# Kernel optimization log

Measured on AMD Instinct MI355X. Metric: run time of the kernel, lower is better.

## Reference

```python
import jax, jax.numpy as jnp
import numpy as np

N = 50000      # number of graph nodes (square sparse matrix)
NNZ = 800000   # nonzeros: avg degree 16
D = 256        # feature dim of m


def setup_inputs() -> dict:
    key = jax.random.key(0)
    k1, k2, k3, k4 = jax.random.split(key, 4)
    m = jax.random.normal(k1, (N, D), dtype=jnp.float32)
    # COO coordinates of the sparse graph matrix; row sorted to mimic CSR layout
    row = jnp.sort(jax.random.randint(k2, (NNZ,), 0, N))
    col = jax.random.randint(k3, (NNZ,), 0, N)
    vals = jax.random.normal(k4, (NNZ,), dtype=jnp.float32)
    return {"m": m, "row": row, "col": col, "vals": vals}


def reference(m, row, col, vals):
    # Faithful to NaiveMerge.forward: cast input to fp16 (self.dtype),
    # SpMM with the fp16 CSR matrix, then cast back to input dtype.
    H = m.astype(jnp.float16)                    # [N, D] fp16
    v = vals.astype(jnp.float16)                 # [NNZ] fp16 (matrix stored in self.dtype)
    msgs = H[col] * v[:, None]                   # [NNZ, D] gathered, scaled messages
    out = jax.ops.segment_sum(msgs, row, num_segments=N)  # CSR row-wise reduce -> [N, D]
    return out.astype(m.dtype)
```

## Files before the change

kernel.cpp:

```cpp
#include <hip/hip_runtime.h>
#include <hip/hip_fp16.h>


#define D   256
#define D4  64
#define D8  32

__device__ __forceinline__ int lower_bound_dev(const int* __restrict__ a, int n, int key) {
    int lo = 0, hi = n;
    while (lo < hi) {
        int mid = (lo + hi) >> 1;
        if (a[mid] < key) lo = mid + 1;
        else hi = mid;
    }
    return lo;
}

__global__ __launch_bounds__(256) void prep_kernel(
        const float4* __restrict__ m4,
        const int* __restrict__ row,
        int nnz, int n_rows,
        uint4* __restrict__ mh_vec,
        int* __restrict__ row_ptr) {
    const int tid = blockIdx.x * blockDim.x + threadIdx.x;
    const int nth = gridDim.x * blockDim.x;

    const int n_items = n_rows * D8;
    for (int i = tid; i < n_items; i += nth) {
        const float4 a = m4[2 * i];
        const float4 b = m4[2 * i + 1];
        union { __half h[8]; uint4 u; } pk;
        pk.h[0] = __float2half(a.x); pk.h[1] = __float2half(a.y);
        pk.h[2] = __float2half(a.z); pk.h[3] = __float2half(a.w);
        pk.h[4] = __float2half(b.x); pk.h[5] = __float2half(b.y);
        pk.h[6] = __float2half(b.z); pk.h[7] = __float2half(b.w);
        mh_vec[i] = pk.u;
    }

    for (int r = tid; r <= n_rows; r += nth) {
        row_ptr[r] = lower_bound_dev(row, nnz, r);
    }
}

__global__ __launch_bounds__(256) void spmm_fp16_kernel(
        const __half* __restrict__ mh,
        const int* __restrict__ row_ptr,
        const int* __restrict__ col,
        const float* __restrict__ vals,
        float4* __restrict__ out4,
        int n_rows) {
    const int wid  = threadIdx.x >> 6;
    const int lane = threadIdx.x & 63;
    const int r = blockIdx.x * 4 + wid;
    if (r >= n_rows) return;

    const int start = __builtin_amdgcn_readfirstlane(row_ptr[r]);
    const int end   = __builtin_amdgcn_readfirstlane(row_ptr[r + 1]);

    const uint2* __restrict__ mh2 = (const uint2*)mh;

    float a0 = 0.f, a1 = 0.f, a2 = 0.f, a3 = 0.f;

    for (int e0 = start; e0 < end; e0 += 16) {
        int   c[16];
        float v[16];
        if (e0 + 16 <= end) {
            #pragma unroll
            for (int j = 0; j < 16; ++j) {
                c[j] = col[e0 + j];
                v[j] = vals[e0 + j];
            }
        } else {
            const int last = end - 1;
            #pragma unroll
            for (int j = 0; j < 16; ++j) {
                const int e  = e0 + j;
                const int ec = e < end ? e : last;
                c[j] = col[ec];
                const float vv = vals[ec];
                v[j] = e < end ? vv : 0.f;
            }
        }

        uint2 g[16];
        #pragma unroll
        for (int j = 0; j < 16; ++j) {
            g[j] = mh2[((size_t)c[j] << 6) + lane];
        }

        __builtin_amdgcn_sched_barrier(0);

        __half2 s01a = __float2half2_rn(0.f);
        __half2 s23a = __float2half2_rn(0.f);
        __half2 s01b = __float2half2_rn(0.f);
        __half2 s23b = __float2half2_rn(0.f);
        #pragma unroll
        for (int j = 0; j < 16; j += 2) {
            const __half2 hva = __float2half2_rn(v[j]);
            s01a = __hfma2(__builtin_bit_cast(__half2, g[j].x), hva, s01a);
            s23a = __hfma2(__builtin_bit_cast(__half2, g[j].y), hva, s23a);
            const __half2 hvb = __float2half2_rn(v[j + 1]);
            s01b = __hfma2(__builtin_bit_cast(__half2, g[j + 1].x), hvb, s01b);
            s23b = __hfma2(__builtin_bit_cast(__half2, g[j + 1].y), hvb, s23b);
        }
        float2 f;
        f = __half22float2(s01a); a0 += f.x; a1 += f.y;
        f = __half22float2(s01b); a0 += f.x; a1 += f.y;
        f = __half22float2(s23a); a2 += f.x; a3 += f.y;
        f = __half22float2(s23b); a2 += f.x; a3 += f.y;
    }

    out4[(size_t)r * D4 + lane] = make_float4(a0, a1, a2, a3);
}

__global__ __launch_bounds__(256) void spmm_fp32_kernel(
        const float4* __restrict__ m4,
        const int* __restrict__ row,
        const int* __restrict__ col,
        const float* __restrict__ vals,
        float4* __restrict__ out4,
        int n_rows, int nnz) {
    const int wid  = threadIdx.x >> 6;
    const int lane = threadIdx.x & 63;
    const int r = blockIdx.x * 4 + wid;
    if (r >= n_rows) return;

    const int start = lower_bound_dev(row, nnz, r);
    const int end   = lower_bound_dev(row, nnz, r + 1);

    float a0 = 0.f, a1 = 0.f, a2 = 0.f, a3 = 0.f;
    for (int e = start; e < end; ++e) {
        const int   c = col[e];
        const float v = vals[e];
        const float4 a = m4[(size_t)c * D4 + lane];
        const __half hv = __float2half(v);
        a0 += __half2float(__hmul(__float2half(a.x), hv));
        a1 += __half2float(__hmul(__float2half(a.y), hv));
        a2 += __half2float(__hmul(__float2half(a.z), hv));
        a3 += __half2float(__hmul(__float2half(a.w), hv));
    }
    out4[(size_t)r * D4 + lane] = make_float4(a0, a1, a2, a3);
}

extern "C" void kernel_launch(void* const* d_in, const int* in_sizes, int n_in,
                              void* d_out, int out_size, void* d_ws, size_t ws_size,
                              hipStream_t stream) {
    const float* m    = (const float*)d_in[0];
    const int*   row  = (const int*)d_in[1];
    const int*   col  = (const int*)d_in[2];
    const float* vals = (const float*)d_in[3];
    float*       out  = (float*)d_out;

    const int nnz    = in_sizes[1];
    const int n_rows = in_sizes[0] / D;

    const size_t mh_bytes = (size_t)n_rows * D * sizeof(__half);
    const size_t rp_bytes = (size_t)(n_rows + 1) * sizeof(int);
    const int blocks = (n_rows + 3) / 4;

    if (ws_size >= mh_bytes + rp_bytes) {
        __half* mh      = (__half*)d_ws;
        int*    row_ptr = (int*)((char*)d_ws + mh_bytes);

        const int n_items = n_rows * D8;
        const int pblocks = (n_items + 255) / 256;
        prep_kernel<<<pblocks, 256, 0, stream>>>(
            (const float4*)m, row, nnz, n_rows, (uint4*)mh, row_ptr);

        spmm_fp16_kernel<<<blocks, 256, 0, stream>>>(
            mh, row_ptr, col, vals, (float4*)out, n_rows);
    } else {
        spmm_fp32_kernel<<<blocks, 256, 0, stream>>>(
            (const float4*)m, row, col, vals, (float4*)out, n_rows, nnz);
    }
}
```

Baseline: 77.60 us.

## Split each wave across two edges with 16-byte gathers and packed col/val

```diff
diff --git a/kernel.cpp b/kernel.cpp
--- a/kernel.cpp
+++ b/kernel.cpp
@@ -5,6 +5,7 @@
 #define D   256
 #define D4  64
 #define D8  32
+#define D16 32
 
 __device__ __forceinline__ int lower_bound_dev(const int* __restrict__ a, int n, int key) {
     int lo = 0, hi = n;
@@ -19,8 +20,11 @@
 __global__ __launch_bounds__(256) void prep_kernel(
         const float4* __restrict__ m4,
         const int* __restrict__ row,
+        const int* __restrict__ col,
+        const float* __restrict__ vals,
         int nnz, int n_rows,
         uint4* __restrict__ mh_vec,
+        int2* __restrict__ cv,
         int* __restrict__ row_ptr) {
     const int tid = blockIdx.x * blockDim.x + threadIdx.x;
     const int nth = gridDim.x * blockDim.x;
@@ -37,9 +41,95 @@
         mh_vec[i] = pk.u;
     }
 
+    for (int e = tid; e < nnz; e += nth) {
+        const __half h = __float2half(vals[e]);
+        const unsigned hu = (unsigned)__builtin_bit_cast(unsigned short, h);
+        int2 t;
+        t.x = col[e];
+        t.y = (int)(hu | (hu << 16));
+        cv[e] = t;
+    }
+
     for (int r = tid; r <= n_rows; r += nth) {
         row_ptr[r] = lower_bound_dev(row, nnz, r);
     }
+}
+
+__global__ __launch_bounds__(256) void spmm_fp16x2_kernel(
+        const uint4* __restrict__ mhv,
+        const int* __restrict__ row_ptr,
+        const int2* __restrict__ cv,
+        float4* __restrict__ out4,
+        int n_rows) {
+    const int wid   = threadIdx.x >> 6;
+    const int lane  = threadIdx.x & 63;
+    const int hlane = lane & 31;
+    const int hi    = lane >> 5;
+    const int r = blockIdx.x * 4 + wid;
+    if (r >= n_rows) return;
+
+    const int start = __builtin_amdgcn_readfirstlane(row_ptr[r]);
+    const int end   = __builtin_amdgcn_readfirstlane(row_ptr[r + 1]);
+
+    float a0 = 0.f, a1 = 0.f, a2 = 0.f, a3 = 0.f;
+    float a4 = 0.f, a5 = 0.f, a6 = 0.f, a7 = 0.f;
+
+    for (int e0 = start; e0 < end; e0 += 32) {
+        int      c[16];
+        unsigned hv[16];
+        if (e0 + 32 <= end) {
+            #pragma unroll
+            for (int j = 0; j < 16; ++j) {
+                const int2 t = cv[e0 + 2 * j + hi];
+                c[j] = t.x; hv[j] = (unsigned)t.y;
+            }
+        } else {
+            const int last = end - 1;
+            #pragma unroll
+            for (int j = 0; j < 16; ++j) {
+                const int e  = e0 + 2 * j + hi;
+                const int ec = e < end ? e : last;
+                const int2 t = cv[ec];
+                c[j] = t.x;
+                hv[j] = e < end ? (unsigned)t.y : 0u;
+            }
+        }
+
+        uint4 g[16];
+        #pragma unroll
+        for (int j = 0; j < 16; ++j) {
+            g[j] = mhv[(size_t)c[j] * D16 + hlane];
+        }
+
+        __builtin_amdgcn_sched_barrier(0);
+
+        __half2 s0 = __float2half2_rn(0.f);
+        __half2 s1 = __float2half2_rn(0.f);
+        __half2 s2 = __float2half2_rn(0.f);
+        __half2 s3 = __float2half2_rn(0.f);
+        #pragma unroll
+        for (int j = 0; j < 16; ++j) {
+            const __half2 hva = __builtin_bit_cast(__half2, hv[j]);
+            s0 = __hfma2(__builtin_bit_cast(__half2, g[j].x), hva, s0);
+            s1 = __hfma2(__builtin_bit_cast(__half2, g[j].y), hva, s1);
+            s2 = __hfma2(__builtin_bit_cast(__half2, g[j].z), hva, s2);
+            s3 = __hfma2(__builtin_bit_cast(__half2, g[j].w), hva, s3);
+        }
+        float2 f;
+        f = __half22float2(s0); a0 += f.x; a1 += f.y;
+        f = __half22float2(s1); a2 += f.x; a3 += f.y;
+        f = __half22float2(s2); a4 += f.x; a5 += f.y;
+        f = __half22float2(s3); a6 += f.x; a7 += f.y;
+    }
+
+    a0 += __shfl_xor(a0, 32); a1 += __shfl_xor(a1, 32);
+    a2 += __shfl_xor(a2, 32); a3 += __shfl_xor(a3, 32);
+    a4 += __shfl_xor(a4, 32); a5 += __shfl_xor(a5, 32);
+    a6 += __shfl_xor(a6, 32); a7 += __shfl_xor(a7, 32);
+
+    const float4 o = hi ? make_float4(a4, a5, a6, a7)
+                        : make_float4(a0, a1, a2, a3);
+    out4[(size_t)r * D4 + hlane * 2 + hi] = o;
 }
 
 __global__ __launch_bounds__(256) void spmm_fp16_kernel(
@@ -56,20 +146,15 @@
 
     const int start = __builtin_amdgcn_readfirstlane(row_ptr[r]);
     const int end   = __builtin_amdgcn_readfirstlane(row_ptr[r + 1]);
-
     const uint2* __restrict__ mh2 = (const uint2*)mh;
 
     float a0 = 0.f, a1 = 0.f, a2 = 0.f, a3 = 0.f;
-
     for (int e0 = start; e0 < end; e0 += 16) {
         int   c[16];
         float v[16];
         if (e0 + 16 <= end) {
             #pragma unroll
-            for (int j = 0; j < 16; ++j) {
-                c[j] = col[e0 + j];
-                v[j] = vals[e0 + j];
-            }
+            for (int j = 0; j < 16; ++j) { c[j] = col[e0 + j]; v[j] = vals[e0 + j]; }
         } else {
             const int last = end - 1;
             #pragma unroll
@@ -81,19 +166,12 @@
                 v[j] = e < end ? vv : 0.f;
             }
         }
-
         uint2 g[16];
         #pragma unroll
-        for (int j = 0; j < 16; ++j) {
-            g[j] = mh2[((size_t)c[j] << 6) + lane];
-        }
-
+        for (int j = 0; j < 16; ++j) g[j] = mh2[((size_t)c[j] << 6) + lane];
         __builtin_amdgcn_sched_barrier(0);
-
-        __half2 s01a = __float2half2_rn(0.f);
-        __half2 s23a = __float2half2_rn(0.f);
-        __half2 s01b = __float2half2_rn(0.f);
-        __half2 s23b = __float2half2_rn(0.f);
+        __half2 s01a = __float2half2_rn(0.f), s23a = __float2half2_rn(0.f);
+        __half2 s01b = __float2half2_rn(0.f), s23b = __float2half2_rn(0.f);
         #pragma unroll
         for (int j = 0; j < 16; j += 2) {
             const __half2 hva = __float2half2_rn(v[j]);
@@ -109,7 +187,6 @@
         f = __half22float2(s23a); a2 += f.x; a3 += f.y;
         f = __half22float2(s23b); a2 += f.x; a3 += f.y;
     }
-
     out4[(size_t)r * D4 + lane] = make_float4(a0, a1, a2, a3);
 }
 
@@ -156,16 +233,31 @@
 
     const size_t mh_bytes = (size_t)n_rows * D * sizeof(__half);
     const size_t rp_bytes = (size_t)(n_rows + 1) * sizeof(int);
+    const size_t cv_bytes = (size_t)nnz * sizeof(int2);
     const int blocks = (n_rows + 3) / 4;
 
-    if (ws_size >= mh_bytes + rp_bytes) {
+    if (ws_size >= mh_bytes + rp_bytes + cv_bytes) {
         __half* mh      = (__half*)d_ws;
         int*    row_ptr = (int*)((char*)d_ws + mh_bytes);
+        int2*   cv      = (int2*)((char*)d_ws + mh_bytes + rp_bytes);
 
         const int n_items = n_rows * D8;
         const int pblocks = (n_items + 255) / 256;
         prep_kernel<<<pblocks, 256, 0, stream>>>(
-            (const float4*)m, row, nnz, n_rows, (uint4*)mh, row_ptr);
+            (const float4*)m, row, col, vals, nnz, n_rows,
+            (uint4*)mh, cv, row_ptr);
+
+        spmm_fp16x2_kernel<<<blocks, 256, 0, stream>>>(
+            (const uint4*)mh, row_ptr, cv, (float4*)out, n_rows);
+    } else if (ws_size >= mh_bytes + rp_bytes) {
+        __half* mh      = (__half*)d_ws;
+        int*    row_ptr = (int*)((char*)d_ws + mh_bytes);
+
+        const int n_items = n_rows * D8;
+        const int pblocks = (n_items + 255) / 256;
+        prep_kernel<<<pblocks, 256, 0, stream>>>(
+            (const float4*)m, row, col, vals, 0 , n_rows,
+            (uint4*)mh, nullptr, row_ptr);
 
         spmm_fp16_kernel<<<blocks, 256, 0, stream>>>(
             mh, row_ptr, col, vals, (float4*)out, n_rows);
```

New measurement: 81.29 us. +4.8%, slower.
